# Kernel tuning notes

Measured on AMD Instinct MI355X. Metric: run time of the kernel, lower is better.

## Reference

```python
import jax, jax.numpy as jnp
import numpy as np

N = 50000          # nodes
E = 1_600_000      # edges (avg degree 32)
D = 128            # in_channels
H = 128            # hidden_channels
B = 4096           # batch_nodes
BETA = 0.5


def setup_inputs() -> dict:
    key = jax.random.key(0)
    ks = jax.random.split(key, 12)
    s = 1.0 / np.sqrt(D)
    inp = {
        "x": jax.random.normal(ks[0], (N, D), jnp.float32),
        "edge_index": jax.random.randint(ks[1], (2, E), 0, N, dtype=jnp.int64),
        "batch_nodes": jax.random.randint(ks[2], (B,), 0, N, dtype=jnp.int64),
        "labels": jax.random.randint(ks[3], (N,), 0, 2, dtype=jnp.int64),
        # GCNConv layer params (weight [in,out], bias [out])
        "W1": jax.random.uniform(ks[4], (D, H), jnp.float32, -s, s),
        "b1": jnp.zeros((H,), jnp.float32),
        "W2": jax.random.uniform(ks[5], (H, H), jnp.float32, -s, s),
        "b2": jnp.zeros((H,), jnp.float32),
        # Bilinear heads: weight [H,H] (out_features=1), scalar bias
        "W_ctx": jax.random.uniform(ks[6], (H, H), jnp.float32, -s, s),
        "b_ctx": jnp.zeros((), jnp.float32),
        "W_loc": jax.random.uniform(ks[7], (H, H), jnp.float32, -s, s),
        "b_loc": jnp.zeros((), jnp.float32),
    }
    return inp


def _gcn_conv(h, W, b, src, dst, n):
    """PyG GCNConv: linear transform, add self-loops, sym-normalized scatter-add."""
    h = h @ W  # [n, out]
    loop = jnp.arange(n, dtype=src.dtype)
    src_f = jnp.concatenate([src, loop])
    dst_f = jnp.concatenate([dst, loop])
    deg = jax.ops.segment_sum(jnp.ones_like(dst_f, dtype=h.dtype), dst_f, num_segments=n)
    dinv = jnp.where(deg > 0, jax.lax.rsqrt(deg), 0.0)
    norm = dinv[src_f] * dinv[dst_f]                      # [E+n]
    msg = h[src_f] * norm[:, None]                        # gather + scale
    out = jax.ops.segment_sum(msg, dst_f, num_segments=n)  # scatter-add
    return out + b


def _bce_logits(z, y):
    # mean(softplus(z) - z*y) == BCEWithLogits
    return jnp.mean(jax.nn.softplus(z) - z * y)


def reference(x, edge_index, batch_nodes, labels, W1, b1, W2, b2, W_ctx, b_ctx, W_loc, b_loc):
    src, dst = edge_index[0], edge_index[1]
    n = x.shape[0]
    layers = [(W1, b1), (W2, b2)]

    # eval mode: dropout is identity
    h = x
    for W, b in layers:
        h = jax.nn.relu(_gcn_conv(h, W, b, src, dst, n))

    gf = h[batch_nodes]                                   # [B, H]
    y = (labels[batch_nodes] == 1).astype(gf.dtype)       # [B]
    pos_cnt = jnp.sum(y)
    neg_cnt = y.shape[0] - pos_cnt
    pos_proto = (y[:, None] * gf).sum(0) / pos_cnt        # [H]

    # context bilinear head: z_i = gf_i^T W_ctx pos_proto + b (neg_sim is dead code in source)
    pos_sim = gf @ (W_ctx @ pos_proto) + b_ctx            # [B]
    ctx_loss = _bce_logits(pos_sim, y)

    # environment view: zero out batch nodes, re-run GCN stack (no dropout in source)
    masked_x = x.at[batch_nodes].set(0.0)
    env_h = masked_x
    for W, b in layers:
        env_h = jax.nn.relu(_gcn_conv(env_h, W, b, src, dst, n))
    env_f = env_h[batch_nodes]                            # [B, H]

    local_sim = jnp.einsum('nd,de,ne->n', env_f, W_loc, gf) + b_loc
    local_loss = _bce_logits(local_sim, 1.0 - y)

    total_loss = BETA * ctx_loss + (1.0 - BETA) * local_loss
    # source's guard: both classes present (true w.h.p. for random labels)
    total_loss = jnp.where((pos_cnt > 0) & (neg_cnt > 0), total_loss, 0.0)
    return gf, total_loss
```

## Files before the change

kernel.cpp:

```cpp
#include <hip/hip_runtime.h>
#include <math.h>

#define HID 128
#define CAP 12288
#define NBUCK_MAX 256
#define EPB 8192

typedef _Float16 h2v __attribute__((ext_vector_type(2)));
typedef _Float16 h8v __attribute__((ext_vector_type(8)));
typedef float f4v __attribute__((ext_vector_type(4)));

static inline int ceil_div(int a, int b) { return (a + b - 1) / b; }


__global__ __launch_bounds__(256) void k_setup(const float* __restrict__ W1, const float* __restrict__ W2,
                                               const float* __restrict__ Wl, _Float16* T1, _Float16* T2,
                                               _Float16* Tl, unsigned int* mask, int* bcur, int mw, int NB) {
    int b = blockIdx.x;
    if (b < 192) {
        int which = b >> 6;
        int idx = (b & 63) * 256 + threadIdx.x;
        int k = idx >> 7, c = idx & 127;
        const float* S = (which == 0) ? W1 : ((which == 1) ? W2 : Wl);
        _Float16* D = (which == 0) ? T1 : ((which == 1) ? T2 : Tl);
        D[c * 128 + k] = (_Float16)S[idx];
    } else {
        int i = (b - 192) * 256 + threadIdx.x;
        if (i < mw) mask[i] = 0u;
        if (i < NB) bcur[i] = i * CAP;
    }
}


__global__ __launch_bounds__(1024) void k_partA(const int* __restrict__ ei, int* __restrict__ bcur,
                                                unsigned int* __restrict__ ebuf,
                                                const int* __restrict__ batch, unsigned int* mask,
                                                int E, int B, int NB, int NBLKE) {
    if ((int)blockIdx.x >= NBLKE) {
        int i = ((int)blockIdx.x - NBLKE) * 1024 + threadIdx.x;
        if (i < B) { int nd = batch[i]; atomicOr(&mask[nd >> 5], 1u << (nd & 31)); }
        return;
    }
    __shared__ int lcnt[NBUCK_MAX];
    __shared__ int sc[NBUCK_MAX];
    __shared__ int lcur[NBUCK_MAX];
    __shared__ int gbase[NBUCK_MAX];
    __shared__ unsigned int se[EPB];
    int tid = threadIdx.x;
    if (tid < NBUCK_MAX) lcnt[tid] = 0;
    __syncthreads();
    int base = blockIdx.x * EPB;
    unsigned int pk[8];
    int bk[8];
#pragma unroll
    for (int j = 0; j < 8; ++j) {
        int e = base + tid + j * 1024;
        if (e < E) {
            int s = ei[e], d = ei[E + e];
            pk[j] = ((unsigned int)s << 8) | (unsigned int)(d & 255);
            bk[j] = d >> 8;
            atomicAdd(&lcnt[bk[j]], 1);
        } else bk[j] = -1;
    }
    __syncthreads();
    if (tid < NBUCK_MAX) sc[tid] = lcnt[tid];
    __syncthreads();
    for (int off = 1; off < NBUCK_MAX; off <<= 1) {
        int v = 0;
        if (tid < NBUCK_MAX && tid >= off) v = sc[tid - off];
        __syncthreads();
        if (tid < NBUCK_MAX) sc[tid] += v;
        __syncthreads();
    }
    if (tid < NBUCK_MAX) {
        int cc = lcnt[tid];
        int lo = sc[tid] - cc;
        lcur[tid] = lo;
        gbase[tid] = cc ? atomicAdd(&bcur[tid], cc) : 0;
    }
    __syncthreads();
#pragma unroll
    for (int j = 0; j < 8; ++j) {
        if (bk[j] >= 0) {
            int r = atomicAdd(&lcur[bk[j]], 1);
            se[r] = pk[j];
        }
    }
    __syncthreads();
    int wid = tid >> 6, lane = tid & 63;
    for (int b = wid; b < NB; b += 16) {
        int cc = lcnt[b];
        int lo = sc[b] - cc;
        int go = gbase[b];
        for (int i = lane; i < cc; i += 64) ebuf[go + i] = se[lo + i];
    }
}


__global__ __launch_bounds__(256) void k_csr(const unsigned int* __restrict__ ebuf, const int* __restrict__ bcur,
                                             const unsigned int* __restrict__ mask, const float* __restrict__ x,
                                             float* __restrict__ sdinv, int* __restrict__ rs,
                                             int* __restrict__ degpk, unsigned int* __restrict__ csr,
                                             _Float16* __restrict__ xs, _Float16* __restrict__ H, int N) {
    __shared__ unsigned int se[CAP];
    __shared__ int deg[256];
    __shared__ int fde[256];
    __shared__ int sc[256];
    __shared__ int cu[256];
    __shared__ int cf[256];
    __shared__ float sda[256];
    int b = blockIdx.x, t = threadIdx.x;
    deg[t] = 0; fde[t] = 0;
    __syncthreads();
    int base = b * CAP;
    int ecnt = bcur[b] - base;
    for (int i = t; i < ecnt; i += 256) {
        unsigned int v = ebuf[base + i];
        int s = v >> 8;
        int fl = (mask[s >> 5] >> (s & 31)) & 1;
        se[i] = ((unsigned int)s << 9) | ((unsigned int)fl << 8) | (v & 255);
        atomicAdd(&deg[v & 255], 1);
        if (fl) atomicAdd(&fde[v & 255], 1);
    }
    __syncthreads();
    int dv = deg[t], fv = fde[t];
    int pv = (dv + 7) & ~7;
    sc[t] = pv;
    __syncthreads();
    for (int off = 1; off < 256; off <<= 1) {
        int v2 = (t >= off) ? sc[t - off] : 0;
        __syncthreads();
        sc[t] += v2;
        __syncthreads();
    }
    int r0 = base + sc[t] - pv;
    cu[t] = r0;
    cf[t] = r0 + (dv - fv);
    int node = b * 256 + t;
    float da = 0.f;
    if (node < N) {
        rs[node] = r0;
        degpk[node] = dv | (fv << 16);
        float di = rsqrtf((float)(dv + 1));
        da = di;
        if ((mask[node >> 5] >> (node & 31)) & 1) di = -di;
        sdinv[node] = di;
    }
    sda[t] = da;
    __syncthreads();
    for (int i = t; i < ecnt; i += 256) {
        unsigned int v = se[i];
        int d8 = v & 255;
        int p = ((v >> 8) & 1) ? atomicAdd(&cf[d8], 1) : atomicAdd(&cu[d8], 1);
        csr[p] = v >> 9;
    }
    if (node < N) {
        for (int j = dv; j < pv; ++j) csr[r0 + j] = (unsigned int)N;
    }
    int nl0 = b * 256;
    int nmax = min(256, N - nl0);
    for (int idx = t; idx < nmax * 16; idx += 256) {
        int nl = idx >> 4, chunk = idx & 15;
        float dda = sda[nl];
        size_t o = (size_t)(nl0 + nl) * HID + chunk * 8;
        float4 a = *(const float4*)&x[o];
        float4 bb = *(const float4*)&x[o + 4];
        h8v v;
        v[0] = (_Float16)(a.x * dda); v[1] = (_Float16)(a.y * dda);
        v[2] = (_Float16)(a.z * dda); v[3] = (_Float16)(a.w * dda);
        v[4] = (_Float16)(bb.x * dda); v[5] = (_Float16)(bb.y * dda);
        v[6] = (_Float16)(bb.z * dda); v[7] = (_Float16)(bb.w * dda);
        *(h8v*)&xs[o] = v;
    }
    if (b == 0) {
        if (t < 16) *(h8v*)&xs[(size_t)N * HID + t * 8] = (h8v){};
        else if (t < 48) *(h8v*)&H[(size_t)2 * N * HID + (t - 16) * 8] = (h8v){};
    }
}


__global__ __launch_bounds__(256) void k_layer1(const _Float16* __restrict__ xs, const int* __restrict__ rs,
                                                const int* __restrict__ degpk, const unsigned int* __restrict__ csr,
                                                const float* __restrict__ sdinv, const _Float16* __restrict__ W1T,
                                                const float* __restrict__ bias, _Float16* __restrict__ H, int N) {
    __shared__ __align__(16) _Float16 sWT[128 * 136];
    __shared__ __align__(16) _Float16 sAgg[32 * 136];
    __shared__ float sbias[128];
    __shared__ float sda[16];
    float* sC = (float*)sWT;

    int tid = threadIdx.x;
    int wave = tid >> 6, lane = tid & 63;
    int grp = lane >> 4, rl = lane & 15;

#pragma unroll
    for (int it = 0; it < 8; ++it) {
        int lin = (it * 256 + tid) * 8;
        int c = lin >> 7, k = lin & 127;
        *(h8v*)&sWT[c * 136 + k] = *(const h8v*)&W1T[lin];
    }
    if (tid < 128) sbias[tid] = bias[tid];
    if (tid < 16) sda[tid] = fabsf(sdinv[blockIdx.x * 16 + tid]);

    int ch = rl * 8;
    int lg = wave * 4 + grp;
    int row = blockIdx.x * 16 + lg;
    bool ok = row < N;
    int p = 0, deg = 0, fd = 0;
    float sd = 0.f;
    h8v hs = {};
    if (ok) {
        p = rs[row];
        int dp = degpk[row];
        deg = dp & 0xffff; fd = dp >> 16;
        sd = sdinv[row];
        hs = *(const h8v*)&xs[(size_t)row * HID + ch];
    }
    int ud = deg - fd;
    int pd = (deg + 7) & ~7;
    int t1 = max(pd, __shfl_xor(pd, 16));
    int m  = max(t1, __shfl_xor(t1, 32));
    float U[8] = {}, F[8] = {};
    for (int i = 0; i < m; i += 16) {
        int id[16];
#pragma unroll
        for (int k = 0; k < 16; ++k) {
            int raw = (int)csr[p + i + k];
            id[k] = (i + k < pd) ? raw : N;
        }
        h8v h[16];
#pragma unroll
        for (int k = 0; k < 16; ++k) h[k] = *(const h8v*)&xs[(size_t)id[k] * HID + ch];
        h8v s0 = (h[0] + h[1]) + (h[2] + h[3]);
        h8v s1 = (h[4] + h[5]) + (h[6] + h[7]);
        h8v s2 = (h[8] + h[9]) + (h[10] + h[11]);
        h8v s3 = (h[12] + h[13]) + (h[14] + h[15]);
        h8v s  = (s0 + s1) + (s2 + s3);
#pragma unroll
        for (int j = 0; j < 8; ++j) U[j] += (float)s[j];
        if (i + 16 > ud) {
#pragma unroll
            for (int k = 0; k < 16; ++k) {
                if (i + k >= ud && i + k < deg) {
#pragma unroll
                    for (int j = 0; j < 8; ++j) F[j] += (float)h[k][j];
                }
            }
        }
    }
    {
        float da = fabsf(sd);
        float keep = (sd < 0.f) ? 0.f : 1.f;
        h8v lo = {}, hi = {};
        if (ok) {
#pragma unroll
            for (int j = 0; j < 8; ++j) {
                float f = (float)hs[j];
                lo[j] = (_Float16)(da * (U[j] + f));
                hi[j] = (_Float16)(da * (U[j] - F[j] + keep * f));
            }
        }
        *(h8v*)&sAgg[(2 * lg) * 136 + ch] = lo;
        *(h8v*)&sAgg[(2 * lg + 1) * 136 + ch] = hi;
    }
    __syncthreads();

    int g = lane >> 4;
    int rowtile = (wave & 1) * 16;
    int colbase = (wave >> 1) * 64;
    f4v acc[4];
#pragma unroll
    for (int cc = 0; cc < 4; ++cc) acc[cc] = (f4v){0.f, 0.f, 0.f, 0.f};
#pragma unroll
    for (int kb = 0; kb < 4; ++kb) {
        int k0 = kb * 32 + g * 8;
        h8v av = *(const h8v*)&sAgg[(rowtile + rl) * 136 + k0];
#pragma unroll
        for (int cc = 0; cc < 4; ++cc) {
            h8v bv = *(const h8v*)&sWT[(colbase + cc * 16 + rl) * 136 + k0];
            acc[cc] = __builtin_amdgcn_mfma_f32_16x16x32_f16(bv, av, acc[cc], 0, 0, 0);
        }
    }
    __syncthreads();

    int lrow = rowtile + rl;
    float dsc = sda[lrow >> 1];
#pragma unroll
    for (int cc = 0; cc < 4; ++cc) {
        f4v v = acc[cc];
        int col = colbase + cc * 16 + g * 4;
#pragma unroll
        for (int i2 = 0; i2 < 4; ++i2) v[i2] = fmaxf(v[i2] + sbias[col + i2], 0.f) * dsc;
        *(f4v*)&sC[lrow * 132 + col] = v;
    }
    __syncthreads();

    int sr = tid >> 3, ck = tid & 7;
    int gRow = blockIdx.x * 32 + sr;
    if (gRow < 2 * N) {
        const float* src = &sC[sr * 132 + ck * 16];
        h8v o0, o1;
#pragma unroll
        for (int j = 0; j < 8; ++j) { o0[j] = (_Float16)src[j]; o1[j] = (_Float16)src[8 + j]; }
        _Float16* dst = &H[(size_t)gRow * HID + ck * 16];
        *(h8v*)&dst[0] = o0;
        *(h8v*)&dst[8] = o1;
    }
}


__global__ __launch_bounds__(256) void k_spmm2(const _Float16* __restrict__ H, const int* __restrict__ rs,
                                               const int* __restrict__ degpk, const unsigned int* __restrict__ csr,
                                               const float* __restrict__ sdinv, const int* __restrict__ batch,
                                               _Float16* __restrict__ aggH2, int B, int N) {
    int wave = threadIdx.x >> 6, lane = threadIdx.x & 63;
    int grp = lane >> 5, rl = lane & 31;
    int ch = rl * 8;
    int ri = blockIdx.x * 8 + wave * 2 + grp;
    bool ok = ri < B;
    int p = 0, deg = 0, row = 0;
    float da = 0.f;
    h8v hs = {};
    if (ok) {
        row = batch[ri];
        p = rs[row];
        deg = degpk[row] & 0xffff;
        da = fabsf(sdinv[row]);
        hs = *(const h8v*)&H[(size_t)row * 256 + ch];
    }
    int pd = (deg + 7) & ~7;
    int m = max(pd, __shfl_xor(pd, 32));
    float a[8] = {};
    for (int i = 0; i < m; i += 16) {
        int id[16];
#pragma unroll
        for (int k = 0; k < 16; ++k) {
            int raw = (int)csr[p + i + k];
            id[k] = (i + k < pd) ? raw : N;
        }
        h8v h[16];
#pragma unroll
        for (int k = 0; k < 16; ++k) h[k] = *(const h8v*)&H[(size_t)id[k] * 256 + ch];
        h8v s0 = (h[0] + h[1]) + (h[2] + h[3]);
        h8v s1 = (h[4] + h[5]) + (h[6] + h[7]);
        h8v s2 = (h[8] + h[9]) + (h[10] + h[11]);
        h8v s3 = (h[12] + h[13]) + (h[14] + h[15]);
        h8v s  = (s0 + s1) + (s2 + s3);
#pragma unroll
        for (int j = 0; j < 8; ++j) a[j] += (float)s[j];
    }
    if (!ok) return;
    h8v o;
#pragma unroll
    for (int j = 0; j < 8; ++j) o[j] = (_Float16)(da * ((float)hs[j] + a[j]));
    *(h8v*)&aggH2[(size_t)ri * 256 + ch] = o;
}


template<int MODE>
__global__ __launch_bounds__(256) void k_gemm(const _Float16* __restrict__ A, const _Float16* __restrict__ WT,
                                              const float* __restrict__ bias,
                                              float* __restrict__ outF, _Float16* __restrict__ outH, int n2) {
    __shared__ __align__(16) char smem[128 * 136 * 2];
    __shared__ float sbias[128];
    _Float16* sWT = (_Float16*)smem;
    float* sC = (float*)smem;
    int tid = threadIdx.x;
#pragma unroll
    for (int it = 0; it < 8; ++it) {
        int lin = (it * 256 + tid) * 8;
        int c = lin >> 7, k = lin & 127;
        *(h8v*)&sWT[c * 136 + k] = *(const h8v*)&WT[lin];
    }
    if (MODE != 2) { if (tid < 128) sbias[tid] = bias[tid]; }
    __syncthreads();

    int wave = tid >> 6, lane = tid & 63;
    int rl = lane & 15, g = lane >> 4;
    int r = blockIdx.x * 64 + wave * 16 + rl;
    bool rok = r < n2;
    f4v acc[8];
#pragma unroll
    for (int cf = 0; cf < 8; ++cf) acc[cf] = (f4v){0.f, 0.f, 0.f, 0.f};
#pragma unroll
    for (int kb = 0; kb < 4; ++kb) {
        int k0 = kb * 32 + g * 8;
        h8v av = {};
        if (rok) av = *(const h8v*)&A[(size_t)r * HID + k0];
#pragma unroll
        for (int cf = 0; cf < 8; ++cf) {
            h8v bv = *(const h8v*)&sWT[(cf * 16 + rl) * 136 + k0];
            acc[cf] = __builtin_amdgcn_mfma_f32_16x16x32_f16(bv, av, acc[cf], 0, 0, 0);
        }
    }
    __syncthreads();
    int lrow = wave * 16 + rl;
#pragma unroll
    for (int cf = 0; cf < 8; ++cf) {
        f4v v = acc[cf];
        if (MODE != 2) {
            int chh = cf * 16 + g * 4;
#pragma unroll
            for (int i2 = 0; i2 < 4; ++i2) v[i2] = fmaxf(v[i2] + sbias[chh + i2], 0.f);
        }
        *(f4v*)&sC[lrow * 132 + cf * 16 + g * 4] = v;
    }
    __syncthreads();
    int lr = tid >> 2, seg = tid & 3;
    int R = blockIdx.x * 64 + lr;
    if (R < n2) {
        const float* src = &sC[lr * 132 + seg * 32];
        if (MODE == 1 && (R & 1) == 0) {
            float* dst = &outF[(size_t)(R >> 1) * HID + seg * 32];
#pragma unroll
            for (int qq = 0; qq < 8; ++qq) *(float4*)&dst[qq * 4] = *(const float4*)&src[qq * 4];
        } else {
            _Float16* dst;
            if (MODE == 1) dst = &outH[(size_t)(R >> 1) * HID + seg * 32];
            else dst = &outH[(size_t)R * HID + seg * 32];
#pragma unroll
            for (int qq = 0; qq < 4; ++qq) {
                h8v o;
#pragma unroll
                for (int j = 0; j < 8; ++j) o[j] = (_Float16)src[qq * 8 + j];
                *(h8v*)&dst[qq * 8] = o;
            }
        }
    }
}


__global__ __launch_bounds__(256) void k_possum(const float* __restrict__ gf, const int* __restrict__ batch,
                                                const int* __restrict__ labels, float* __restrict__ yv,
                                                float* __restrict__ part, float* __restrict__ pos_part) {
    __shared__ float s[256];
    __shared__ float sy[256];
    int t = threadIdx.x;
    int r0 = blockIdx.x * 256;
    int b = r0 + t;
    float y = (labels[batch[b]] == 1) ? 1.f : 0.f;
    yv[b] = y;
    sy[t] = y;
    __syncthreads();
    int ch = t & 127, half = t >> 7;
    float acc = 0.f;
    for (int r = half; r < 256; r += 2) acc += sy[r] * gf[(size_t)(r0 + r) * HID + ch];
    s[t] = acc;
    __syncthreads();
    if (t < 128) part[blockIdx.x * 128 + t] = s[t] + s[t + 128];
    __syncthreads();
    s[t] = sy[t];
    __syncthreads();
    for (int st = 128; st > 0; st >>= 1) {
        if (t < st) s[t] += s[t + st];
        __syncthreads();
    }
    if (t == 0) pos_part[blockIdx.x] = s[0];
}

__global__ __launch_bounds__(128) void k_ctxvec(const float* __restrict__ Wctx, const float* __restrict__ part,
                                                const float* __restrict__ pos_part, float* v, float* pcnt) {
    __shared__ float sproto[128];
    __shared__ float spc;
    int t = threadIdx.x;
    if (t == 0) {
        float pc = 0.f;
        for (int i = 0; i < 16; ++i) pc += pos_part[i];
        spc = pc;
        pcnt[0] = pc;
    }
    float ssum = 0.f;
    for (int i = 0; i < 16; ++i) ssum += part[i * 128 + t];
    __syncthreads();
    sproto[t] = ssum / spc;
    __syncthreads();
    float acc = 0.f;
#pragma unroll 4
    for (int j = 0; j < 128; ++j) acc += Wctx[t * 128 + j] * sproto[j];
    v[t] = acc;
}

__global__ __launch_bounds__(256) void k_heads(const float* __restrict__ gf, const _Float16* __restrict__ T,
                                               const float* __restrict__ v, const float* __restrict__ yv,
                                               const float* __restrict__ bctx, const float* __restrict__ bloc,
                                               float* pA, float* pB, int B) {
    int wave = threadIdx.x >> 6, lane = threadIdx.x & 63;
    int b = blockIdx.x * 4 + wave;
    if (b >= B) return;
    float2 g = *(const float2*)&gf[(size_t)b * HID + lane * 2];
    h2v tt = *(const h2v*)&T[(size_t)b * HID + lane * 2];
    float2 vv = *(const float2*)&v[lane * 2];
    float s1 = g.x * vv.x + g.y * vv.y;
    float s2 = g.x * (float)tt[0] + g.y * (float)tt[1];
    for (int o = 32; o > 0; o >>= 1) {
        s1 += __shfl_xor(s1, o);
        s2 += __shfl_xor(s2, o);
    }
    if (lane == 0) {
        float y = yv[b];
        float z1 = s1 + bctx[0];
        float z2 = s2 + bloc[0];
        pA[b] = fmaxf(z1, 0.f) + log1pf(expf(-fabsf(z1))) - z1 * y;
        pB[b] = fmaxf(z2, 0.f) + log1pf(expf(-fabsf(z2))) - z2 * (1.f - y);
    }
}

__global__ __launch_bounds__(256) void k_final(const float* __restrict__ pA, const float* __restrict__ pB,
                                               const float* __restrict__ pcnt, float* out_loss, int B) {
    __shared__ float s1[256];
    __shared__ float s2[256];
    int t = threadIdx.x;
    float a = 0.f, b2 = 0.f;
    for (int i = t; i < B; i += 256) { a += pA[i]; b2 += pB[i]; }
    s1[t] = a;
    s2[t] = b2;
    __syncthreads();
    for (int st = 128; st > 0; st >>= 1) {
        if (t < st) { s1[t] += s1[t + st]; s2[t] += s2[t + st]; }
        __syncthreads();
    }
    if (t == 0) {
        float pc = pcnt[0];
        float nc = (float)B - pc;
        float total = 0.5f * (s1[0] / (float)B) + 0.5f * (s2[0] / (float)B);
        out_loss[0] = (pc > 0.f && nc > 0.f) ? total : 0.f;
    }
}


extern "C" void kernel_launch(void* const* d_in, const int* in_sizes, int n_in,
                              void* d_out, int out_size, void* d_ws, size_t ws_size,
                              hipStream_t stream) {
    const float* x      = (const float*)d_in[0];
    const int*   ei     = (const int*)d_in[1];
    const int*   batch  = (const int*)d_in[2];
    const int*   labels = (const int*)d_in[3];
    const float* W1     = (const float*)d_in[4];
    const float* b1     = (const float*)d_in[5];
    const float* W2     = (const float*)d_in[6];
    const float* b2     = (const float*)d_in[7];
    const float* Wctx   = (const float*)d_in[8];
    const float* bctx   = (const float*)d_in[9];
    const float* Wloc   = (const float*)d_in[10];
    const float* bloc   = (const float*)d_in[11];

    int N = in_sizes[0] / HID;
    int E = in_sizes[1] / 2;
    int B = in_sizes[2];
    float* out = (float*)d_out;

    char* wsb = (char*)d_ws;
    size_t off = 0;
    auto alloc = [&](size_t bytes) -> char* {
        char* p = wsb + off;
        off += (bytes + 255) & ~(size_t)255;
        return p;
    };
    int NB = ceil_div(N, 256);
    int mw = ceil_div(N, 32);

    _Float16* xs   = (_Float16*)alloc((size_t)(N + 1) * HID * 2);
    _Float16* H    = (_Float16*)alloc((size_t)(2 * N + 2) * HID * 2);
    unsigned int* ebuf = (unsigned int*)alloc((size_t)NB * CAP * 4);
    unsigned int* csr  = (unsigned int*)alloc((size_t)NB * CAP * 4);
    float* sdinv = (float*)alloc((size_t)N * 4);
    int*   rs    = (int*)alloc((size_t)N * 4);
    int*   degpk = (int*)alloc((size_t)N * 4);
    int*   bcur  = (int*)alloc((size_t)NB * 4);
    unsigned int* mask = (unsigned int*)alloc((size_t)mw * 4);
    _Float16* W1T = (_Float16*)alloc(128 * 128 * 2);
    _Float16* W2T = (_Float16*)alloc(128 * 128 * 2);
    _Float16* WlT = (_Float16*)alloc(128 * 128 * 2);
    _Float16* aggH2 = (_Float16*)alloc((size_t)B * 256 * 2);
    _Float16* envh  = (_Float16*)alloc((size_t)B * HID * 2);
    _Float16* Tt    = (_Float16*)alloc((size_t)B * HID * 2);
    float* yv   = (float*)alloc((size_t)B * 4);
    float* pos_part = (float*)alloc(64 * 4);
    float* part     = (float*)alloc(16 * 128 * 4);
    float* vvec     = (float*)alloc(128 * 4);
    float* pcnt     = (float*)alloc(256);
    float* pA       = (float*)alloc((size_t)B * 4);
    float* pB       = (float*)alloc((size_t)B * 4);
    (void)ws_size; (void)n_in; (void)out_size;

    int NBLKE = ceil_div(E, EPB);
    int NBLKB = ceil_div(B, 1024);

    k_setup<<<192 + ceil_div(mw, 256), 256, 0, stream>>>(W1, W2, Wloc, W1T, W2T, WlT, mask, bcur, mw, NB);

    k_partA<<<NBLKE + NBLKB, 1024, 0, stream>>>(ei, bcur, ebuf, batch, mask, E, B, NB, NBLKE);

    k_csr<<<NB, 256, 0, stream>>>(ebuf, bcur, mask, x, sdinv, rs, degpk, csr, xs, H, N);

    k_layer1<<<ceil_div(N, 16), 256, 0, stream>>>(xs, rs, degpk, csr, sdinv, W1T, b1, H, N);

    k_spmm2<<<ceil_div(B, 8), 256, 0, stream>>>(H, rs, degpk, csr, sdinv, batch, aggH2, B, N);
    k_gemm<1><<<ceil_div(2 * B, 64), 256, 0, stream>>>(aggH2, W2T, b2, out, envh, 2 * B);

    k_gemm<2><<<ceil_div(B, 64), 256, 0, stream>>>(envh, WlT, nullptr, nullptr, Tt, B);

    k_possum<<<16, 256, 0, stream>>>(out, batch, labels, yv, part, pos_part);
    k_ctxvec<<<1, 128, 0, stream>>>(Wctx, part, pos_part, vvec, pcnt);
    k_heads<<<ceil_div(B, 4), 256, 0, stream>>>(out, Tt, vvec, yv, bctx, bloc, pA, pB, B);
    k_final<<<1, 256, 0, stream>>>(pA, pB, pcnt, out + (size_t)B * HID, B);
}
```

Before: 180.1 us.

## Fuse layer-2 batch aggregation with W2 GEMM into single kernel

Merges the batch-row sparse aggregation (k_spmm2) and the layer-2 GEMM with bias+ReLU into one kernel, k_layer2. Aggregated rows are staged in shared memory instead of a global aggH2 buffer, and the mode-2 GEMM is split out into a simplified k_gemmT. Each 16-lane group now gathers both the normal and env halves of a row in 8-neighbor chunks rather than 16. This removes a launch and a global round trip, but each block reloads W2 into LDS for only 16 rows and uses more shared memory, which may lower occupancy.

```diff
diff --git a/kernel.cpp b/kernel.cpp
--- a/kernel.cpp
+++ b/kernel.cpp
@@ -309,60 +309,131 @@
 }
 
 
-__global__ __launch_bounds__(256) void k_spmm2(const _Float16* __restrict__ H, const int* __restrict__ rs,
-                                               const int* __restrict__ degpk, const unsigned int* __restrict__ csr,
-                                               const float* __restrict__ sdinv, const int* __restrict__ batch,
-                                               _Float16* __restrict__ aggH2, int B, int N) {
-    int wave = threadIdx.x >> 6, lane = threadIdx.x & 63;
-    int grp = lane >> 5, rl = lane & 31;
+__global__ __launch_bounds__(256) void k_layer2(const _Float16* __restrict__ H, const int* __restrict__ rs,
+                                                const int* __restrict__ degpk, const unsigned int* __restrict__ csr,
+                                                const float* __restrict__ sdinv, const int* __restrict__ batch,
+                                                const _Float16* __restrict__ W2T, const float* __restrict__ bias,
+                                                float* __restrict__ gf, _Float16* __restrict__ envh, int B, int N) {
+    __shared__ __align__(16) _Float16 sWT[128 * 136];
+    __shared__ __align__(16) _Float16 sAgg[32 * 136];
+    __shared__ float sbias[128];
+    float* sC = (float*)sWT;
+
+    int tid = threadIdx.x;
+    int wave = tid >> 6, lane = tid & 63;
+    int grp = lane >> 4, rl = lane & 15;
+
+#pragma unroll
+    for (int it = 0; it < 8; ++it) {
+        int lin = (it * 256 + tid) * 8;
+        int c = lin >> 7, k = lin & 127;
+        *(h8v*)&sWT[c * 136 + k] = *(const h8v*)&W2T[lin];
+    }
+    if (tid < 128) sbias[tid] = bias[tid];
+
     int ch = rl * 8;
-    int ri = blockIdx.x * 8 + wave * 2 + grp;
+    int lg = wave * 4 + grp;
+    int ri = blockIdx.x * 16 + lg;
     bool ok = ri < B;
     int p = 0, deg = 0, row = 0;
     float da = 0.f;
-    h8v hs = {};
+    h8v hn = {}, he = {};
     if (ok) {
         row = batch[ri];
         p = rs[row];
         deg = degpk[row] & 0xffff;
         da = fabsf(sdinv[row]);
-        hs = *(const h8v*)&H[(size_t)row * 256 + ch];
+        hn = *(const h8v*)&H[(size_t)row * 256 + ch];
+        he = *(const h8v*)&H[(size_t)row * 256 + 128 + ch];
     }
     int pd = (deg + 7) & ~7;
-    int m = max(pd, __shfl_xor(pd, 32));
-    float a[8] = {};
-    for (int i = 0; i < m; i += 16) {
-        int id[16];
-#pragma unroll
-        for (int k = 0; k < 16; ++k) {
+    int t1 = max(pd, __shfl_xor(pd, 16));
+    int m  = max(t1, __shfl_xor(t1, 32));
+    float a[8] = {}, e[8] = {};
+    for (int i = 0; i < m; i += 8) {
+        int id[8];
+#pragma unroll
+        for (int k = 0; k < 8; ++k) {
             int raw = (int)csr[p + i + k];
             id[k] = (i + k < pd) ? raw : N;
         }
-        h8v h[16];
-#pragma unroll
-        for (int k = 0; k < 16; ++k) h[k] = *(const h8v*)&H[(size_t)id[k] * 256 + ch];
-        h8v s0 = (h[0] + h[1]) + (h[2] + h[3]);
-        h8v s1 = (h[4] + h[5]) + (h[6] + h[7]);
-        h8v s2 = (h[8] + h[9]) + (h[10] + h[11]);
-        h8v s3 = (h[12] + h[13]) + (h[14] + h[15]);
-        h8v s  = (s0 + s1) + (s2 + s3);
-#pragma unroll
-        for (int j = 0; j < 8; ++j) a[j] += (float)s[j];
-    }
-    if (!ok) return;
-    h8v o;
-#pragma unroll
-    for (int j = 0; j < 8; ++j) o[j] = (_Float16)(da * ((float)hs[j] + a[j]));
-    *(h8v*)&aggH2[(size_t)ri * 256 + ch] = o;
-}
-
-
-template<int MODE>
-__global__ __launch_bounds__(256) void k_gemm(const _Float16* __restrict__ A, const _Float16* __restrict__ WT,
-                                              const float* __restrict__ bias,
-                                              float* __restrict__ outF, _Float16* __restrict__ outH, int n2) {
+        h8v xn[8], xe[8];
+#pragma unroll
+        for (int k = 0; k < 8; ++k) {
+            xn[k] = *(const h8v*)&H[(size_t)id[k] * 256 + ch];
+            xe[k] = *(const h8v*)&H[(size_t)id[k] * 256 + 128 + ch];
+        }
+        h8v sn = ((xn[0] + xn[1]) + (xn[2] + xn[3])) + ((xn[4] + xn[5]) + (xn[6] + xn[7]));
+        h8v sv = ((xe[0] + xe[1]) + (xe[2] + xe[3])) + ((xe[4] + xe[5]) + (xe[6] + xe[7]));
+#pragma unroll
+        for (int j = 0; j < 8; ++j) { a[j] += (float)sn[j]; e[j] += (float)sv[j]; }
+    }
+    {
+        h8v lo = {}, hi = {};
+        if (ok) {
+#pragma unroll
+            for (int j = 0; j < 8; ++j) {
+                lo[j] = (_Float16)(da * (a[j] + (float)hn[j]));
+                hi[j] = (_Float16)(da * (e[j] + (float)he[j]));
+            }
+        }
+        *(h8v*)&sAgg[(2 * lg) * 136 + ch] = lo;
+        *(h8v*)&sAgg[(2 * lg + 1) * 136 + ch] = hi;
+    }
+    __syncthreads();
+
+    int g = lane >> 4;
+    int rowtile = (wave & 1) * 16;
+    int colbase = (wave >> 1) * 64;
+    f4v acc[4];
+#pragma unroll
+    for (int cc = 0; cc < 4; ++cc) acc[cc] = (f4v){0.f, 0.f, 0.f, 0.f};
+#pragma unroll
+    for (int kb = 0; kb < 4; ++kb) {
+        int k0 = kb * 32 + g * 8;
+        h8v av = *(const h8v*)&sAgg[(rowtile + rl) * 136 + k0];
+#pragma unroll
+        for (int cc = 0; cc < 4; ++cc) {
+            h8v bv = *(const h8v*)&sWT[(colbase + cc * 16 + rl) * 136 + k0];
+            acc[cc] = __builtin_amdgcn_mfma_f32_16x16x32_f16(bv, av, acc[cc], 0, 0, 0);
+        }
+    }
+    __syncthreads();
+
+    int lrow = rowtile + rl;
+#pragma unroll
+    for (int cc = 0; cc < 4; ++cc) {
+        f4v v = acc[cc];
+        int col = colbase + cc * 16 + g * 4;
+#pragma unroll
+        for (int i2 = 0; i2 < 4; ++i2) v[i2] = fmaxf(v[i2] + sbias[col + i2], 0.f);
+        *(f4v*)&sC[lrow * 132 + col] = v;
+    }
+    __syncthreads();
+
+    int sr = tid >> 3, ck = tid & 7;
+    int ri2 = blockIdx.x * 16 + (sr >> 1);
+    if (ri2 < B) {
+        const float* src = &sC[sr * 132 + ck * 16];
+        if ((sr & 1) == 0) {
+            float* dst = &gf[(size_t)ri2 * HID + ck * 16];
+#pragma unroll
+            for (int q = 0; q < 4; ++q) *(float4*)&dst[q * 4] = *(const float4*)&src[q * 4];
+        } else {
+            h8v o0, o1;
+#pragma unroll
+            for (int j = 0; j < 8; ++j) { o0[j] = (_Float16)src[j]; o1[j] = (_Float16)src[8 + j]; }
+            _Float16* dst = &envh[(size_t)ri2 * HID + ck * 16];
+            *(h8v*)&dst[0] = o0;
+            *(h8v*)&dst[8] = o1;
+        }
+    }
+}
+
+
+__global__ __launch_bounds__(256) void k_gemmT(const _Float16* __restrict__ A, const _Float16* __restrict__ WT,
+                                               _Float16* __restrict__ outH, int n2) {
     __shared__ __align__(16) char smem[128 * 136 * 2];
-    __shared__ float sbias[128];
     _Float16* sWT = (_Float16*)smem;
     float* sC = (float*)smem;
     int tid = threadIdx.x;
@@ -372,7 +443,6 @@
         int c = lin >> 7, k = lin & 127;
         *(h8v*)&sWT[c * 136 + k] = *(const h8v*)&WT[lin];
     }
-    if (MODE != 2) { if (tid < 128) sbias[tid] = bias[tid]; }
     __syncthreads();
 
     int wave = tid >> 6, lane = tid & 63;
@@ -397,34 +467,20 @@
     int lrow = wave * 16 + rl;
 #pragma unroll
     for (int cf = 0; cf < 8; ++cf) {
-        f4v v = acc[cf];
-        if (MODE != 2) {
-            int chh = cf * 16 + g * 4;
-#pragma unroll
-            for (int i2 = 0; i2 < 4; ++i2) v[i2] = fmaxf(v[i2] + sbias[chh + i2], 0.f);
-        }
-        *(f4v*)&sC[lrow * 132 + cf * 16 + g * 4] = v;
+        *(f4v*)&sC[lrow * 132 + cf * 16 + g * 4] = acc[cf];
     }
     __syncthreads();
     int lr = tid >> 2, seg = tid & 3;
     int R = blockIdx.x * 64 + lr;
     if (R < n2) {
         const float* src = &sC[lr * 132 + seg * 32];
-        if (MODE == 1 && (R & 1) == 0) {
-            float* dst = &outF[(size_t)(R >> 1) * HID + seg * 32];
-#pragma unroll
-            for (int qq = 0; qq < 8; ++qq) *(float4*)&dst[qq * 4] = *(const float4*)&src[qq * 4];
-        } else {
-            _Float16* dst;
-            if (MODE == 1) dst = &outH[(size_t)(R >> 1) * HID + seg * 32];
-            else dst = &outH[(size_t)R * HID + seg * 32];
-#pragma unroll
-            for (int qq = 0; qq < 4; ++qq) {
-                h8v o;
-#pragma unroll
-                for (int j = 0; j < 8; ++j) o[j] = (_Float16)src[qq * 8 + j];
-                *(h8v*)&dst[qq * 8] = o;
-            }
+        _Float16* dst = &outH[(size_t)R * HID + seg * 32];
+#pragma unroll
+        for (int qq = 0; qq < 4; ++qq) {
+            h8v o;
+#pragma unroll
+            for (int j = 0; j < 8; ++j) o[j] = (_Float16)src[qq * 8 + j];
+            *(h8v*)&dst[qq * 8] = o;
         }
     }
 }
@@ -571,7 +627,6 @@
     _Float16* W1T = (_Float16*)alloc(128 * 128 * 2);
     _Float16* W2T = (_Float16*)alloc(128 * 128 * 2);
     _Float16* WlT = (_Float16*)alloc(128 * 128 * 2);
-    _Float16* aggH2 = (_Float16*)alloc((size_t)B * 256 * 2);
     _Float16* envh  = (_Float16*)alloc((size_t)B * HID * 2);
     _Float16* Tt    = (_Float16*)alloc((size_t)B * HID * 2);
     float* yv   = (float*)alloc((size_t)B * 4);
@@ -587,17 +642,14 @@
     int NBLKB = ceil_div(B, 1024);
 
     k_setup<<<192 + ceil_div(mw, 256), 256, 0, stream>>>(W1, W2, Wloc, W1T, W2T, WlT, mask, bcur, mw, NB);
-
     k_partA<<<NBLKE + NBLKB, 1024, 0, stream>>>(ei, bcur, ebuf, batch, mask, E, B, NB, NBLKE);
-
     k_csr<<<NB, 256, 0, stream>>>(ebuf, bcur, mask, x, sdinv, rs, degpk, csr, xs, H, N);
 
     k_layer1<<<ceil_div(N, 16), 256, 0, stream>>>(xs, rs, degpk, csr, sdinv, W1T, b1, H, N);
 
-    k_spmm2<<<ceil_div(B, 8), 256, 0, stream>>>(H, rs, degpk, csr, sdinv, batch, aggH2, B, N);
-    k_gemm<1><<<ceil_div(2 * B, 64), 256, 0, stream>>>(aggH2, W2T, b2, out, envh, 2 * B);
-
-    k_gemm<2><<<ceil_div(B, 64), 256, 0, stream>>>(envh, WlT, nullptr, nullptr, Tt, B);
+    k_layer2<<<ceil_div(B, 16), 256, 0, stream>>>(H, rs, degpk, csr, sdinv, batch, W2T, b2, out, envh, B, N);
+
+    k_gemmT<<<ceil_div(B, 64), 256, 0, stream>>>(envh, WlT, Tt, B);
 
     k_possum<<<16, 256, 0, stream>>>(out, batch, labels, yv, part, pos_part);
     k_ctxvec<<<1, 128, 0, stream>>>(Wctx, part, pos_part, vvec, pcnt);
```

Result: no change. 176.5 us (-2.0%).
